# Kernel optimization log

Measured on AMD Instinct MI355X. Metric: run time of the kernel, lower is better.

Reference implementation:

```python
import jax, jax.numpy as jnp
import numpy as np

B, T, D = 1, 8192, 1024
H, DH = 16, 64
WIN = 128          # attention window (tokens on each side)
WB = 128
NB = T // WB
EPS = 1e-5


def _layernorm(x, g, b):
    mu = jnp.mean(x, axis=-1, keepdims=True)
    var = jnp.mean(jnp.square(x - mu), axis=-1, keepdims=True)
    return (x - mu) * jax.lax.rsqrt(var + EPS) * g + b


def _band_mask():
    # query offset i in [0, WB), key offset j in [0, 3*WB) within [prev|self|next] blocks
    i = jnp.arange(WB)[:, None]
    j = jnp.arange(3 * WB)[None, :]
    rel = j - WB - i                      # key_pos - query_pos
    band = jnp.abs(rel) <= WIN            # sliding window |i-j| <= W (matches torch mask)
    blk = jnp.arange(NB)[:, None, None]
    key_pos = blk * WB + (j - WB)[None]   # absolute key position
    return band[None] & (key_pos >= 0) & (key_pos < T)   # [NB, WB, 3*WB]


def _local_attention(q, k, v):
    # q,k,v: [B,H,T,DH] -> block-local SDPA, mathematically identical to
    # full SDPA with the additive band mask in the torch code.
    def blocks(t):
        return t.reshape(B, H, NB, WB, DH)
    qb = blocks(q)
    kp = jnp.pad(blocks(k), ((0, 0), (0, 0), (1, 1), (0, 0), (0, 0)))
    vp = jnp.pad(blocks(v), ((0, 0), (0, 0), (1, 1), (0, 0), (0, 0)))
    # gather [prev, self, next] key/value blocks: [B,H,NB,3*WB,DH]
    k3 = jnp.concatenate([kp[:, :, s:s + NB] for s in range(3)], axis=3)
    v3 = jnp.concatenate([vp[:, :, s:s + NB] for s in range(3)], axis=3)
    scores = jnp.einsum('bhnqd,bhnkd->bhnqk', qb, k3) / np.sqrt(DH).astype(np.float32)
    mask = _band_mask()                                   # [NB,WB,3WB]
    scores = jnp.where(mask[None, None], scores, -jnp.inf)
    attn = jax.nn.softmax(scores, axis=-1)
    out = jnp.einsum('bhnqk,bhnkd->bhnqd', attn, v3)      # [B,H,NB,WB,DH]
    return out.reshape(B, H, T, DH)


def setup_inputs() -> dict:
    key = jax.random.key(0)
    ks = jax.random.split(key, 7)
    s = 0.02
    return {
        'x': jax.random.normal(ks[0], (B, T, D), jnp.float32),
        'wq': jax.random.normal(ks[1], (D, D), jnp.float32) * s,
        'wk': jax.random.normal(ks[2], (D, D), jnp.float32) * s,
        'wv': jax.random.normal(ks[3], (D, D), jnp.float32) * s,
        'wo': jax.random.normal(ks[4], (D, D), jnp.float32) * s,
        'wg': jax.random.normal(ks[5], (D, 2 * D), jnp.float32) * s,
        'wd': jax.random.normal(ks[6], (2 * D, D), jnp.float32) * s,
        'norm_g': jnp.ones((D,), jnp.float32),
        'norm_b': jnp.zeros((D,), jnp.float32),
        'ffn_g': jnp.ones((D,), jnp.float32),
        'ffn_b': jnp.zeros((D,), jnp.float32),
    }


def reference(x, wq, wk, wv, wo, wg, wd, norm_g, norm_b, ffn_g, ffn_b):
    h = _layernorm(x, norm_g, norm_b)
    def heads(t):  # [B,T,D] -> [B,H,T,DH]
        return t.reshape(B, T, H, DH).transpose(0, 2, 1, 3)
    q, k, v = heads(h @ wq), heads(h @ wk), heads(h @ wv)
    attn_out = _local_attention(q, k, v)                     # [B,H,T,DH]
    attn_out = attn_out.transpose(0, 2, 1, 3).reshape(B, T, D)
    x = x + attn_out @ wo
    h = _layernorm(x, ffn_g, ffn_b)
    x = x + jax.nn.silu(h @ wg) @ wd
    return x
```

## Files before the change

### kernel.cpp

```cpp
#include <hip/hip_runtime.h>
#include <cstdint>

#define T_DIM 8192
#define D_DIM 1024
#define NB_DIM 64
#define QKS 2048

typedef __bf16 bf16x8 __attribute__((ext_vector_type(8)));
typedef __bf16 bf16x4 __attribute__((ext_vector_type(4)));
typedef float f32x4 __attribute__((ext_vector_type(4)));

#define MFMA16(a, b, c) __builtin_amdgcn_mfma_f32_16x16x32_bf16((a), (b), (c), 0, 0, 0)
#define BAR() asm volatile("s_barrier" ::: "memory")
#define VMCNT(n) asm volatile("s_waitcnt vmcnt(" #n ")" ::: "memory")

__device__ __forceinline__ void gld_lds16(const void* gsrc, void* ldst) {
  __builtin_amdgcn_global_load_lds(
      (__attribute__((address_space(1))) void*)(uintptr_t)gsrc,
      (__attribute__((address_space(3))) void*)(uintptr_t)ldst,
      16, 0, 0);
}

__global__ __launch_bounds__(256) void transpose_cvt(
    const float* __restrict__ W, __bf16* __restrict__ Wt, int K, int N) {
  __shared__ float tile[32][33];
  const int tx = threadIdx.x & 31, ty = threadIdx.x >> 5;
  const int n0 = blockIdx.x * 32, k0 = blockIdx.y * 32;
#pragma unroll
  for (int i = 0; i < 32; i += 8)
    tile[ty + i][tx] = W[(size_t)(k0 + ty + i) * N + n0 + tx];
  __syncthreads();
#pragma unroll
  for (int i = 0; i < 32; i += 8)
    Wt[(size_t)(n0 + ty + i) * K + k0 + tx] = (__bf16)tile[tx][ty + i];
}

template <typename TI>
__global__ __launch_bounds__(256) void ln_kernel(
    const TI* __restrict__ x, const float* __restrict__ g,
    const float* __restrict__ b, __bf16* __restrict__ out) {
  __shared__ float red[8];
  const int row = blockIdx.x, tid = threadIdx.x;
  float v0, v1, v2, v3;
  if constexpr (sizeof(TI) == 4) {
    const float4 v = ((const float4*)(x + (size_t)row * D_DIM))[tid];
    v0 = v.x; v1 = v.y; v2 = v.z; v3 = v.w;
  } else {
    const bf16x4 v = ((const bf16x4*)(x + (size_t)row * D_DIM))[tid];
    v0 = (float)v[0]; v1 = (float)v[1]; v2 = (float)v[2]; v3 = (float)v[3];
  }
  float s = v0 + v1 + v2 + v3;
#pragma unroll
  for (int off = 32; off >= 1; off >>= 1) s += __shfl_xor(s, off, 64);
  if ((tid & 63) == 0) red[tid >> 6] = s;
  __syncthreads();
  const float mean = (red[0] + red[1] + red[2] + red[3]) * (1.0f / D_DIM);
  const float d0 = v0 - mean, d1 = v1 - mean, d2 = v2 - mean, d3 = v3 - mean;
  float ss = d0 * d0 + d1 * d1 + d2 * d2 + d3 * d3;
#pragma unroll
  for (int off = 32; off >= 1; off >>= 1) ss += __shfl_xor(ss, off, 64);
  if ((tid & 63) == 0) red[4 + (tid >> 6)] = ss;
  __syncthreads();
  const float var = (red[4] + red[5] + red[6] + red[7]) * (1.0f / D_DIM);
  const float rstd = rsqrtf(var + 1e-5f);
  const float4 gg = ((const float4*)g)[tid];
  const float4 bb = ((const float4*)b)[tid];
  bf16x4 o;
  o[0] = (__bf16)(d0 * rstd * gg.x + bb.x);
  o[1] = (__bf16)(d1 * rstd * gg.y + bb.y);
  o[2] = (__bf16)(d2 * rstd * gg.z + bb.z);
  o[3] = (__bf16)(d3 * rstd * gg.w + bb.w);
  *(bf16x4*)(out + (size_t)row * D_DIM + tid * 4) = o;
}

__global__ __launch_bounds__(256, 2) void gemm_vt(
    const __bf16* __restrict__ A, const __bf16* __restrict__ Bt,
    __bf16* __restrict__ Cout, int M, int N, int K) {
  __shared__ __bf16 smem[32768];
  __bf16* As = smem;
  __bf16* Bs = smem + 16384;
  const int tid = threadIdx.x;
  const int l = tid & 63, w = tid >> 6;
  const int lr = l & 15, lg = l >> 4;
  const int wr = w >> 1, wc = w & 1;
  const int bm = blockIdx.y, bn = blockIdx.x;
  const size_t arow0 = (size_t)bm * 128;
  const size_t brow0 = (size_t)bn * 128;

  f32x4 acc[4][4];
  const f32x4 z4 = {0.f, 0.f, 0.f, 0.f};
#pragma unroll
  for (int m = 0; m < 4; ++m)
#pragma unroll
    for (int n = 0; n < 4; ++n) acc[m][n] = z4;

  auto stage = [&](int buf, int k0) {
#pragma unroll
    for (int r = 0; r < 4; ++r) {
      int ci = r * 256 + tid;
      int row = ci >> 3, c8 = ci & 7;
      gld_lds16(A + (arow0 + row) * K + k0 + c8 * 8, &As[buf * 8192 + ci * 8]);
    }
#pragma unroll
    for (int r = 0; r < 4; ++r) {
      int ci = r * 256 + tid;
      int row = ci >> 3, c8 = ci & 7;
      gld_lds16(Bt + (brow0 + row) * K + k0 + c8 * 8, &Bs[buf * 8192 + ci * 8]);
    }
  };

  stage(0, 0);
  const int nk = K >> 6;
  int cur = 0;
  __syncthreads();

  for (int t = 0; t < nk; ++t) {
    if (t + 1 < nk) stage(cur ^ 1, (t + 1) << 6);
#pragma unroll
    for (int kk = 0; kk < 2; ++kk) {
      bf16x8 af[4], bf_[4];
#pragma unroll
      for (int m = 0; m < 4; ++m)
        af[m] = *(const bf16x8*)&As[cur * 8192 + (wr * 64 + m * 16 + lr) * 64 + kk * 32 + lg * 8];
#pragma unroll
      for (int n = 0; n < 4; ++n)
        bf_[n] = *(const bf16x8*)&Bs[cur * 8192 + (wc * 64 + n * 16 + lr) * 64 + kk * 32 + lg * 8];
#pragma unroll
      for (int m = 0; m < 4; ++m)
#pragma unroll
        for (int n = 0; n < 4; ++n) acc[m][n] = MFMA16(af[m], bf_[n], acc[m][n]);
    }
    __syncthreads();
    cur ^= 1;
  }

  __bf16* Tt = smem;
#pragma unroll
  for (int m = 0; m < 4; ++m)
#pragma unroll
    for (int n = 0; n < 4; ++n)
#pragma unroll
      for (int r = 0; r < 4; ++r)
        Tt[(wc * 64 + n * 16 + lr) * 136 + wr * 64 + m * 16 + lg * 4 + r] =
            (__bf16)acc[m][n][r];
  __syncthreads();
#pragma unroll
  for (int i = 0; i < 8; ++i) {
    const int ci = i * 256 + tid;
    const int c = ci >> 4;
    const int rr = (ci & 15) * 8;
    const bf16x8 vv = *(const bf16x8*)&Tt[c * 136 + rr];
    *(bf16x8*)(Cout + (size_t)(bn * 128 + c) * M + bm * 128 + rr) = vv;
  }
}

template <int BM_, int EPI>
__global__ __launch_bounds__(512, 2) void gemm8(
    const __bf16* __restrict__ A, const __bf16* __restrict__ Bt,
    const void* __restrict__ Res, void* __restrict__ Cout,
    int M, int N, int K, int nbn) {
  constexpr int MF = BM_ / 32;
  constexpr int MH = MF / 2;
  constexpr int SA = 8 * MF;
  constexpr int LA = BM_ / 128;
  constexpr int ATILE = BM_ * 64;
  constexpr int AHALF = BM_ * 32;
  constexpr int BOFF = 2 * ATILE;
  __shared__ __bf16 lds[2 * BM_ * 64 + 32768];

  const int tid = threadIdx.x;
  const int l = tid & 63, w = tid >> 6;
  const int lr = l & 15, lg = l >> 4;
  const int wr = w >> 2, wc = w & 3;
  const int nwg = gridDim.x;
  const int bid = (int)blockIdx.x;
  const int swz = (bid & 7) * (nwg >> 3) + (bid >> 3);
  const int bm = swz / nbn, bn = swz % nbn;
  const int am0 = bm * BM_, bn0 = bn * 256;

  f32x4 acc[MF][4];
  const f32x4 z4 = {0.f, 0.f, 0.f, 0.f};
#pragma unroll
  for (int m = 0; m < MF; ++m)
#pragma unroll
    for (int n = 0; n < 4; ++n) acc[m][n] = z4;

  auto stageA = [&](int h, int b, int k0) {
#pragma unroll
    for (int r = 0; r < LA; ++r) {
      const int ci = r * 512 + tid;
      const int wri = ci >> 3, c8 = ci & 7;
      const int ra = (wri % SA) + (wri / SA) * (2 * SA) + h * SA;
      gld_lds16(A + (size_t)(am0 + ra) * K + k0 + ((c8 ^ (wri & 7)) << 3),
                (__bf16*)lds + b * ATILE + h * AHALF + ci * 8);
    }
  };
  auto stageB = [&](int h, int b, int k0) {
#pragma unroll
    for (int r = 0; r < 2; ++r) {
      const int ci = r * 512 + tid;
      const int wri = ci >> 3, c8 = ci & 7;
      const int rb = (wri & 31) + (wri >> 5) * 64 + h * 32;
      gld_lds16(Bt + (size_t)(bn0 + rb) * K + k0 + ((c8 ^ (wri & 7)) << 3),
                (__bf16*)lds + BOFF + b * 16384 + h * 8192 + ci * 8);
    }
  };

  const int x7 = lr & 7;
  const int aoff0 = (lr + wr * SA) * 64 + ((lg) ^ x7) * 8;
  const int aoff1 = (lr + wr * SA) * 64 + ((4 + lg) ^ x7) * 8;
  const int boff0 = BOFF + (lr + wc * 32) * 64 + ((lg) ^ x7) * 8;
  const int boff1 = BOFF + (lr + wc * 32) * 64 + ((4 + lg) ^ x7) * 8;

  const int nt = K >> 6;
  stageA(0, 0, 0);
  stageB(1, 0, 0);
  stageB(0, 0, 0);
  stageA(1, 0, 0);
  stageA(0, 1, 64);
  stageB(1, 1, 64);
  if constexpr (BM_ == 256) VMCNT(6); else VMCNT(4);
  BAR();

  int buf = 0;
  bf16x8 afr[MH][2], bfr0[2][2], bfr1[2][2];
  for (int t = 0; t < nt; ++t) {
    const bool s1 = (t + 1 < nt);
    const bool s2 = (t + 2 < nt);
    const int nb = buf ^ 1;
    const int k1 = (t + 1) << 6;
    const int k2 = (t + 2) << 6;
    const __bf16* pa0 = lds + buf * ATILE + aoff0;
    const __bf16* pa1 = lds + buf * ATILE + aoff1;
    const __bf16* pb0 = lds + buf * 16384 + boff0;
    const __bf16* pb1 = lds + buf * 16384 + boff1;

#pragma unroll
    for (int i = 0; i < MH; ++i) {
      afr[i][0] = *(const bf16x8*)(pa0 + i * 1024);
      afr[i][1] = *(const bf16x8*)(pa1 + i * 1024);
    }
#pragma unroll
    for (int j = 0; j < 2; ++j) {
      bfr0[j][0] = *(const bf16x8*)(pb0 + j * 1024);
      bfr0[j][1] = *(const bf16x8*)(pb1 + j * 1024);
    }
    if (s1) stageB(0, nb, k1);
    BAR();
    __builtin_amdgcn_s_setprio(1);
#pragma unroll
    for (int kk = 0; kk < 2; ++kk)
#pragma unroll
      for (int i = 0; i < MH; ++i)
#pragma unroll
        for (int j = 0; j < 2; ++j)
          acc[i][j] = MFMA16(afr[i][kk], bfr0[j][kk], acc[i][j]);
    __builtin_amdgcn_s_setprio(0);

#pragma unroll
    for (int j = 0; j < 2; ++j) {
      bfr1[j][0] = *(const bf16x8*)(pb0 + 8192 + j * 1024);
      bfr1[j][1] = *(const bf16x8*)(pb1 + 8192 + j * 1024);
    }
    if (s1) {
      stageA(1, nb, k1);
      if constexpr (BM_ == 256) VMCNT(8); else VMCNT(6);
    } else {
      VMCNT(0);
    }
    BAR();
    __builtin_amdgcn_s_setprio(1);
#pragma unroll
    for (int kk = 0; kk < 2; ++kk)
#pragma unroll
      for (int i = 0; i < MH; ++i)
#pragma unroll
        for (int j = 0; j < 2; ++j)
          acc[i][2 + j] = MFMA16(afr[i][kk], bfr1[j][kk], acc[i][2 + j]);
    __builtin_amdgcn_s_setprio(0);

#pragma unroll
    for (int i = 0; i < MH; ++i) {
      afr[i][0] = *(const bf16x8*)(pa0 + AHALF + i * 1024);
      afr[i][1] = *(const bf16x8*)(pa1 + AHALF + i * 1024);
    }
    if (s2) stageA(0, buf, k2);
    BAR();
    __builtin_amdgcn_s_setprio(1);
#pragma unroll
    for (int kk = 0; kk < 2; ++kk)
#pragma unroll
      for (int i = 0; i < MH; ++i)
#pragma unroll
        for (int j = 0; j < 2; ++j)
          acc[MH + i][2 + j] = MFMA16(afr[i][kk], bfr1[j][kk], acc[MH + i][2 + j]);
    __builtin_amdgcn_s_setprio(0);

    if (s2) {
      stageB(1, buf, k2);
      if constexpr (BM_ == 256) VMCNT(6); else VMCNT(4);
    } else if (s1) {
      if constexpr (BM_ == 256) VMCNT(2); else VMCNT(1);
    }
    BAR();
    __builtin_amdgcn_s_setprio(1);
#pragma unroll
    for (int kk = 0; kk < 2; ++kk)
#pragma unroll
      for (int i = 0; i < MH; ++i)
#pragma unroll
        for (int j = 0; j < 2; ++j)
          acc[MH + i][j] = MFMA16(afr[i][kk], bfr0[j][kk], acc[MH + i][j]);
    __builtin_amdgcn_s_setprio(0);

    buf = nb;
  }

  if constexpr (EPI == 5) {
    const __bf16* R = (const __bf16*)Res;
    float* O = (float*)Cout;
#pragma unroll
    for (int mf = 0; mf < MF; ++mf)
#pragma unroll
      for (int nf = 0; nf < 4; ++nf)
#pragma unroll
        for (int r = 0; r < 4; ++r) {
          const int row = am0 + wr * 2 * SA + mf * 16 + lg * 4 + r;
          const int col = bn0 + wc * 64 + nf * 16 + lr;
          const size_t idx = (size_t)row * N + col;
          O[idx] = acc[mf][nf][r] + (float)R[idx];
        }
  } else {
    __syncthreads();
    __bf16* Ct = (__bf16*)lds;
#pragma unroll
    for (int mf = 0; mf < MF; ++mf)
#pragma unroll
      for (int nf = 0; nf < 4; ++nf)
#pragma unroll
        for (int r = 0; r < 4; ++r) {
          const int rl = wr * 2 * SA + mf * 16 + lg * 4 + r;
          const int cl = wc * 64 + nf * 16 + lr;
          float v = acc[mf][nf][r];
          if constexpr (EPI == 3) v = v / (1.f + __expf(-v));
          if constexpr (EPI == 4)
            v += ((const float*)Res)[(size_t)(am0 + rl) * N + bn0 + cl];
          Ct[rl * 256 + (((cl >> 3) ^ (rl & 7)) << 3) + (cl & 7)] = (__bf16)v;
        }
    __syncthreads();
    __bf16* O = (__bf16*)Cout;
#pragma unroll
    for (int i = 0; i < BM_ / 16; ++i) {
      const int ci = i * 512 + tid;
      const int row = ci >> 5, c8 = ci & 31;
      *(bf16x8*)(O + (size_t)(am0 + row) * N + bn0 + c8 * 8) =
          *(const bf16x8*)&Ct[row * 256 + ((c8 ^ (row & 7)) << 3)];
    }
  }
}

__global__ __launch_bounds__(256, 2) void attn_kernel(
    const __bf16* __restrict__ qk, const __bf16* __restrict__ vT,
    __bf16* __restrict__ out) {
  __shared__ __bf16 Pl[4][32 * 136];

  const int tid = threadIdx.x;
  const int l = tid & 63, w = tid >> 6;
  const int lr = l & 15, lg = l >> 4;
  const int bx = (int)blockIdx.x;
  const int swz = (bx & 7) * 128 + (bx >> 3);
  const int h = swz >> 6;
  const int blk = swz & 63;
  __bf16* Pw = Pl[w];

  const __bf16* qbase =
      qk + (size_t)(blk * 128 + w * 32 + lr) * QKS + h * 64 + lg * 8;
  bf16x8 qf[2][2];
#pragma unroll
  for (int m = 0; m < 2; ++m)
#pragma unroll
    for (int ks = 0; ks < 2; ++ks)
      qf[m][ks] = *(const bf16x8*)(qbase + (size_t)m * 16 * QKS + ks * 32);

  const f32x4 z4 = {0.f, 0.f, 0.f, 0.f};
  float ssum[2][4];
  f32x4 o[2][4];
#pragma unroll
  for (int m = 0; m < 2; ++m) {
#pragma unroll
    for (int r = 0; r < 4; ++r) ssum[m][r] = 0.f;
#pragma unroll
    for (int n = 0; n < 4; ++n) o[m][n] = z4;
  }

  for (int it = 0; it < 3; ++it) {
    const int kb = blk + it - 1;
    if (kb < 0 || kb >= NB_DIM) continue;
    const int rel = it - 1;
    const int kclo = (rel < 0) ? (w * 2) : 0;
    const int kchi = (rel > 0) ? (w * 2 + 2) : 8;

    f32x4 s[2][8];
    const __bf16* kbase =
        qk + (size_t)(kb * 128 + lr) * QKS + 1024 + h * 64 + lg * 8;
#pragma unroll
    for (int kc = 0; kc < 8; ++kc) {
      if (kc < kclo || kc >= kchi) continue;
      const bf16x8 k0 = *(const bf16x8*)(kbase + (size_t)kc * 16 * QKS);
      const bf16x8 k1 = *(const bf16x8*)(kbase + (size_t)kc * 16 * QKS + 32);
      s[0][kc] = MFMA16(qf[0][0], k0, z4);
      s[1][kc] = MFMA16(qf[1][0], k0, z4);
      s[0][kc] = MFMA16(qf[0][1], k1, s[0][kc]);
      s[1][kc] = MFMA16(qf[1][1], k1, s[1][kc]);
    }

#pragma unroll
    for (int m = 0; m < 2; ++m) {
#pragma unroll
      for (int r = 0; r < 4; ++r) {
        const int qi = w * 32 + m * 16 + lg * 4 + r;
        float acc_s = 0.f;
#pragma unroll
        for (int kc = 0; kc < 8; ++kc) {
          if (kc < kclo || kc >= kchi) continue;
          const int kj = kc * 16 + lr;
          float p = __expf(s[m][kc][r] * 0.125f);
          const bool valid = (rel == 0) || (rel < 0 ? (kj >= qi) : (kj <= qi));
          p = valid ? p : 0.f;
          s[m][kc][r] = p;
          acc_s += p;
        }
        ssum[m][r] += acc_s;
      }
    }

#pragma unroll
    for (int m = 0; m < 2; ++m)
#pragma unroll
      for (int kc = 0; kc < 8; ++kc) {
        if (kc < kclo || kc >= kchi) continue;
#pragma unroll
        for (int r = 0; r < 4; ++r)
          Pw[(m * 16 + lg * 4 + r) * 136 + kc * 16 + lr] = (__bf16)s[m][kc][r];
      }

    const int kslo = kclo >> 1, kshi = kchi >> 1;
    const __bf16* vbase =
        vT + (size_t)(h * 64 + lr) * T_DIM + kb * 128 + lg * 8;
#pragma unroll
    for (int ks = 0; ks < 4; ++ks) {
      if (ks < kslo || ks >= kshi) continue;
      bf16x8 pa[2];
#pragma unroll
      for (int m = 0; m < 2; ++m)
        pa[m] = *(const bf16x8*)&Pw[(m * 16 + lr) * 136 + ks * 32 + lg * 8];
#pragma unroll
      for (int n = 0; n < 4; ++n) {
        const bf16x8 vb = *(const bf16x8*)(vbase + (size_t)n * 16 * T_DIM + ks * 32);
        o[0][n] = MFMA16(pa[0], vb, o[0][n]);
        o[1][n] = MFMA16(pa[1], vb, o[1][n]);
      }
    }
  }

  float inv[2][4];
#pragma unroll
  for (int m = 0; m < 2; ++m)
#pragma unroll
    for (int r = 0; r < 4; ++r) {
      float rs = ssum[m][r];
#pragma unroll
      for (int off = 1; off < 16; off <<= 1) rs += __shfl_xor(rs, off, 64);
      inv[m][r] = __builtin_amdgcn_rcpf(rs);
    }
#pragma unroll
  for (int m = 0; m < 2; ++m)
#pragma unroll
    for (int n = 0; n < 4; ++n)
#pragma unroll
      for (int r = 0; r < 4; ++r)
        Pw[(m * 16 + lg * 4 + r) * 136 + n * 16 + lr] =
            (__bf16)(o[m][n][r] * inv[m][r]);
#pragma unroll
  for (int i = 0; i < 4; ++i) {
    const int ci = i * 64 + l;
    const int qrow = ci >> 3;
    const int c8 = (ci & 7) * 8;
    const bf16x8 vv = *(const bf16x8*)&Pw[qrow * 136 + c8];
    *(bf16x8*)(out + (size_t)(blk * 128 + w * 32 + qrow) * D_DIM + h * 64 + c8) = vv;
  }
}

extern "C" void kernel_launch(void* const* d_in, const int* in_sizes, int n_in,
                              void* d_out, int out_size, void* d_ws, size_t ws_size,
                              hipStream_t stream) {
  (void)in_sizes; (void)n_in; (void)out_size; (void)ws_size;
  const float* x      = (const float*)d_in[0];
  const float* wq     = (const float*)d_in[1];
  const float* wk     = (const float*)d_in[2];
  const float* wv     = (const float*)d_in[3];
  const float* wo     = (const float*)d_in[4];
  const float* wg     = (const float*)d_in[5];
  const float* wd     = (const float*)d_in[6];
  const float* norm_g = (const float*)d_in[7];
  const float* norm_b = (const float*)d_in[8];
  const float* ffn_g  = (const float*)d_in[9];
  const float* ffn_b  = (const float*)d_in[10];
  float* out = (float*)d_out;

  char* ws = (char*)d_ws;
  constexpr size_t MB = 1ull << 20;
  __bf16* wqkT = (__bf16*)(ws + 0 * MB);
  __bf16* wvT  = (__bf16*)(ws + 4 * MB);
  __bf16* woT  = (__bf16*)(ws + 6 * MB);
  __bf16* wgT  = (__bf16*)(ws + 8 * MB);
  __bf16* wdT  = (__bf16*)(ws + 12 * MB);
  __bf16* hbuf = (__bf16*)(ws + 16 * MB);
  __bf16* qkbf = (__bf16*)(ws + 32 * MB);
  __bf16* gbf  = (__bf16*)(ws + 32 * MB);
  __bf16* vTbf = (__bf16*)(ws + 64 * MB);
  __bf16* x2bf = (__bf16*)(ws + 80 * MB);

  transpose_cvt<<<dim3(32, 32), 256, 0, stream>>>(wq, wqkT, 1024, 1024);
  transpose_cvt<<<dim3(32, 32), 256, 0, stream>>>(wk, wqkT + 1024 * 1024, 1024, 1024);
  transpose_cvt<<<dim3(32, 32), 256, 0, stream>>>(wv, wvT, 1024, 1024);
  transpose_cvt<<<dim3(32, 32), 256, 0, stream>>>(wo, woT, 1024, 1024);
  transpose_cvt<<<dim3(64, 32), 256, 0, stream>>>(wg, wgT, 1024, 2048);
  transpose_cvt<<<dim3(32, 64), 256, 0, stream>>>(wd, wdT, 2048, 1024);

  ln_kernel<float><<<8192, 256, 0, stream>>>(x, norm_g, norm_b, hbuf);

  gemm8<256, 0><<<256, 512, 0, stream>>>(hbuf, wqkT, nullptr, qkbf, 8192, 2048, 1024, 8);
  gemm_vt<<<dim3(8, 64), 256, 0, stream>>>(hbuf, wvT, vTbf, 8192, 1024, 1024);

  attn_kernel<<<1024, 256, 0, stream>>>(qkbf, vTbf, hbuf);

  gemm8<128, 4><<<256, 512, 0, stream>>>(hbuf, woT, x, x2bf, 8192, 1024, 1024, 4);

  ln_kernel<__bf16><<<8192, 256, 0, stream>>>(x2bf, ffn_g, ffn_b, hbuf);

  gemm8<256, 3><<<256, 512, 0, stream>>>(hbuf, wgT, nullptr, gbf, 8192, 2048, 1024, 8);

  gemm8<128, 5><<<256, 512, 0, stream>>>(gbf, wdT, x2bf, out, 8192, 1024, 2048, 4);
}
```

Before: 255.4 us.

## Fuse weight transposes into one launch and split wide GEMMs into BM=128 halves

Replaces six weight transpose-convert launches with one kernel that picks the source matrix from the block index. Drops the BM=256 GEMM variant: the QK and gate projections (N=2048) now run as two BM=128 launches over column halves, with a separate output leading dimension. This cuts launch overhead and the 256-row tile's register and LDS pressure, at the cost of an extra launch per wide GEMM and less A-tile reuse across N.

Measured after the change: 259.8 us. No clear change (+1.7%).

```diff
diff --git a/kernel.cpp b/kernel.cpp
--- a/kernel.cpp
+++ b/kernel.cpp
@@ -21,11 +21,25 @@
       16, 0, 0);
 }
 
-__global__ __launch_bounds__(256) void transpose_cvt(
-    const float* __restrict__ W, __bf16* __restrict__ Wt, int K, int N) {
+__global__ __launch_bounds__(256) void transpose_all(
+    const float* __restrict__ wq, const float* __restrict__ wk,
+    const float* __restrict__ wv, const float* __restrict__ wo,
+    const float* __restrict__ wg, const float* __restrict__ wd,
+    __bf16* __restrict__ wqkT, __bf16* __restrict__ wvT,
+    __bf16* __restrict__ woT, __bf16* __restrict__ wgT,
+    __bf16* __restrict__ wdT) {
   __shared__ float tile[32][33];
+  const int bid = (int)blockIdx.x;
+  const float* W; __bf16* Wt; int K, N, n0, k0, local;
+  if (bid < 1024)      { W = wq; Wt = wqkT;            K = 1024; N = 1024; local = bid; }
+  else if (bid < 2048) { W = wk; Wt = wqkT + 1048576;  K = 1024; N = 1024; local = bid - 1024; }
+  else if (bid < 3072) { W = wv; Wt = wvT;             K = 1024; N = 1024; local = bid - 2048; }
+  else if (bid < 4096) { W = wo; Wt = woT;             K = 1024; N = 1024; local = bid - 3072; }
+  else if (bid < 6144) { W = wg; Wt = wgT;             K = 1024; N = 2048; local = bid - 4096; }
+  else                 { W = wd; Wt = wdT;             K = 2048; N = 1024; local = bid - 6144; }
+  if (N == 2048) { n0 = (local & 63) * 32; k0 = (local >> 6) * 32; }
+  else           { n0 = (local & 31) * 32; k0 = (local >> 5) * 32; }
   const int tx = threadIdx.x & 31, ty = threadIdx.x >> 5;
-  const int n0 = blockIdx.x * 32, k0 = blockIdx.y * 32;
 #pragma unroll
   for (int i = 0; i < 32; i += 8)
     tile[ty + i][tx] = W[(size_t)(k0 + ty + i) * N + n0 + tx];
@@ -154,11 +168,12 @@
   }
 }
 
-template <int BM_, int EPI>
+template <int EPI>
 __global__ __launch_bounds__(512, 2) void gemm8(
     const __bf16* __restrict__ A, const __bf16* __restrict__ Bt,
     const void* __restrict__ Res, void* __restrict__ Cout,
-    int M, int N, int K, int nbn) {
+    int M, int K, int nbn, int ldc) {
+  constexpr int BM_ = 128;
   constexpr int MF = BM_ / 32;
   constexpr int MH = MF / 2;
   constexpr int SA = 8 * MF;
@@ -219,7 +234,7 @@
   stageA(1, 0, 0);
   stageA(0, 1, 64);
   stageB(1, 1, 64);
-  if constexpr (BM_ == 256) VMCNT(6); else VMCNT(4);
+  VMCNT(4);
   BAR();
 
   int buf = 0;
@@ -264,7 +279,7 @@
     }
     if (s1) {
       stageA(1, nb, k1);
-      if constexpr (BM_ == 256) VMCNT(8); else VMCNT(6);
+      VMCNT(6);
     } else {
       VMCNT(0);
     }
@@ -298,9 +313,9 @@
 
     if (s2) {
       stageB(1, buf, k2);
-      if constexpr (BM_ == 256) VMCNT(6); else VMCNT(4);
+      VMCNT(4);
     } else if (s1) {
-      if constexpr (BM_ == 256) VMCNT(2); else VMCNT(1);
+      VMCNT(1);
     }
     BAR();
     __builtin_amdgcn_s_setprio(1);
@@ -327,7 +342,7 @@
         for (int r = 0; r < 4; ++r) {
           const int row = am0 + wr * 2 * SA + mf * 16 + lg * 4 + r;
           const int col = bn0 + wc * 64 + nf * 16 + lr;
-          const size_t idx = (size_t)row * N + col;
+          const size_t idx = (size_t)row * ldc + col;
           O[idx] = acc[mf][nf][r] + (float)R[idx];
         }
   } else {
@@ -344,7 +359,7 @@
           float v = acc[mf][nf][r];
           if constexpr (EPI == 3) v = v / (1.f + __expf(-v));
           if constexpr (EPI == 4)
-            v += ((const float*)Res)[(size_t)(am0 + rl) * N + bn0 + cl];
+            v += ((const float*)Res)[(size_t)(am0 + rl) * D_DIM + bn0 + cl];
           Ct[rl * 256 + (((cl >> 3) ^ (rl & 7)) << 3) + (cl & 7)] = (__bf16)v;
         }
     __syncthreads();
@@ -353,7 +368,7 @@
     for (int i = 0; i < BM_ / 16; ++i) {
       const int ci = i * 512 + tid;
       const int row = ci >> 5, c8 = ci & 31;
-      *(bf16x8*)(O + (size_t)(am0 + row) * N + bn0 + c8 * 8) =
+      *(bf16x8*)(O + (size_t)(am0 + row) * ldc + bn0 + c8 * 8) =
           *(const bf16x8*)&Ct[row * 256 + ((c8 ^ (row & 7)) << 3)];
     }
   }
@@ -521,25 +536,27 @@
   __bf16* vTbf = (__bf16*)(ws + 64 * MB);
   __bf16* x2bf = (__bf16*)(ws + 80 * MB);
 
-  transpose_cvt<<<dim3(32, 32), 256, 0, stream>>>(wq, wqkT, 1024, 1024);
-  transpose_cvt<<<dim3(32, 32), 256, 0, stream>>>(wk, wqkT + 1024 * 1024, 1024, 1024);
-  transpose_cvt<<<dim3(32, 32), 256, 0, stream>>>(wv, wvT, 1024, 1024);
-  transpose_cvt<<<dim3(32, 32), 256, 0, stream>>>(wo, woT, 1024, 1024);
-  transpose_cvt<<<dim3(64, 32), 256, 0, stream>>>(wg, wgT, 1024, 2048);
-  transpose_cvt<<<dim3(32, 64), 256, 0, stream>>>(wd, wdT, 2048, 1024);
+  transpose_all<<<8192, 256, 0, stream>>>(wq, wk, wv, wo, wg, wd,
+                                          wqkT, wvT, woT, wgT, wdT);
 
   ln_kernel<float><<<8192, 256, 0, stream>>>(x, norm_g, norm_b, hbuf);
 
-  gemm8<256, 0><<<256, 512, 0, stream>>>(hbuf, wqkT, nullptr, qkbf, 8192, 2048, 1024, 8);
+  gemm8<0><<<256, 512, 0, stream>>>(hbuf, wqkT, nullptr, qkbf,
+                                    8192, 1024, 4, 2048);
+  gemm8<0><<<256, 512, 0, stream>>>(hbuf, wqkT + 1024 * 1024, nullptr, qkbf + 1024,
+                                    8192, 1024, 4, 2048);
   gemm_vt<<<dim3(8, 64), 256, 0, stream>>>(hbuf, wvT, vTbf, 8192, 1024, 1024);
 
   attn_kernel<<<1024, 256, 0, stream>>>(qkbf, vTbf, hbuf);
 
-  gemm8<128, 4><<<256, 512, 0, stream>>>(hbuf, woT, x, x2bf, 8192, 1024, 1024, 4);
+  gemm8<4><<<256, 512, 0, stream>>>(hbuf, woT, x, x2bf, 8192, 1024, 4, 1024);
 
   ln_kernel<__bf16><<<8192, 256, 0, stream>>>(x2bf, ffn_g, ffn_b, hbuf);
 
-  gemm8<256, 3><<<256, 512, 0, stream>>>(hbuf, wgT, nullptr, gbf, 8192, 2048, 1024, 8);
-
-  gemm8<128, 5><<<256, 512, 0, stream>>>(gbf, wdT, x2bf, out, 8192, 1024, 2048, 4);
-}
+  gemm8<3><<<256, 512, 0, stream>>>(hbuf, wgT, nullptr, gbf,
+                                    8192, 1024, 4, 2048);
+  gemm8<3><<<256, 512, 0, stream>>>(hbuf, wgT + 1024 * 1024, nullptr, gbf + 1024,
+                                    8192, 1024, 4, 2048);
+
+  gemm8<5><<<256, 512, 0, stream>>>(gbf, wdT, x2bf, out, 8192, 2048, 4, 1024);
+}
```

## Merge weight transposes into one launch and compute V^T via gemm8 with swapped operands

Applied to the files above, without the earlier changes.

Six separate transpose_cvt launches become a single transpose_all kernel that dispatches on block index, which cuts launch overhead. The dedicated gemm_vt kernel, which transposed V through LDS in its epilogue, is removed. V^T is now produced by the existing tuned gemm8<128,0> kernel, computing Wv^T·h^T by passing wvT as A and hbuf as Bt. This reuses the faster 512-thread GEMM path, but relies on gemm8 handling M=1024 and N=8192 with 32 column blocks correctly.

After: 245.4 us. 1.04x faster.

```diff
diff --git a/kernel.cpp b/kernel.cpp
--- a/kernel.cpp
+++ b/kernel.cpp
@@ -21,11 +21,25 @@
       16, 0, 0);
 }
 
-__global__ __launch_bounds__(256) void transpose_cvt(
-    const float* __restrict__ W, __bf16* __restrict__ Wt, int K, int N) {
+__global__ __launch_bounds__(256) void transpose_all(
+    const float* __restrict__ wq, const float* __restrict__ wk,
+    const float* __restrict__ wv, const float* __restrict__ wo,
+    const float* __restrict__ wg, const float* __restrict__ wd,
+    __bf16* __restrict__ wqkT, __bf16* __restrict__ wvT,
+    __bf16* __restrict__ woT, __bf16* __restrict__ wgT,
+    __bf16* __restrict__ wdT) {
   __shared__ float tile[32][33];
+  const int bid = (int)blockIdx.x;
+  const float* W; __bf16* Wt; int K, N, n0, k0, local;
+  if (bid < 1024)      { W = wq; Wt = wqkT;            K = 1024; N = 1024; local = bid; }
+  else if (bid < 2048) { W = wk; Wt = wqkT + 1048576;  K = 1024; N = 1024; local = bid - 1024; }
+  else if (bid < 3072) { W = wv; Wt = wvT;             K = 1024; N = 1024; local = bid - 2048; }
+  else if (bid < 4096) { W = wo; Wt = woT;             K = 1024; N = 1024; local = bid - 3072; }
+  else if (bid < 6144) { W = wg; Wt = wgT;             K = 1024; N = 2048; local = bid - 4096; }
+  else                 { W = wd; Wt = wdT;             K = 2048; N = 1024; local = bid - 6144; }
+  if (N == 2048) { n0 = (local & 63) * 32; k0 = (local >> 6) * 32; }
+  else           { n0 = (local & 31) * 32; k0 = (local >> 5) * 32; }
   const int tx = threadIdx.x & 31, ty = threadIdx.x >> 5;
-  const int n0 = blockIdx.x * 32, k0 = blockIdx.y * 32;
 #pragma unroll
   for (int i = 0; i < 32; i += 8)
     tile[ty + i][tx] = W[(size_t)(k0 + ty + i) * N + n0 + tx];
@@ -71,87 +85,6 @@
   o[2] = (__bf16)(d2 * rstd * gg.z + bb.z);
   o[3] = (__bf16)(d3 * rstd * gg.w + bb.w);
   *(bf16x4*)(out + (size_t)row * D_DIM + tid * 4) = o;
-}
-
-__global__ __launch_bounds__(256, 2) void gemm_vt(
-    const __bf16* __restrict__ A, const __bf16* __restrict__ Bt,
-    __bf16* __restrict__ Cout, int M, int N, int K) {
-  __shared__ __bf16 smem[32768];
-  __bf16* As = smem;
-  __bf16* Bs = smem + 16384;
-  const int tid = threadIdx.x;
-  const int l = tid & 63, w = tid >> 6;
-  const int lr = l & 15, lg = l >> 4;
-  const int wr = w >> 1, wc = w & 1;
-  const int bm = blockIdx.y, bn = blockIdx.x;
-  const size_t arow0 = (size_t)bm * 128;
-  const size_t brow0 = (size_t)bn * 128;
-
-  f32x4 acc[4][4];
-  const f32x4 z4 = {0.f, 0.f, 0.f, 0.f};
-#pragma unroll
-  for (int m = 0; m < 4; ++m)
-#pragma unroll
-    for (int n = 0; n < 4; ++n) acc[m][n] = z4;
-
-  auto stage = [&](int buf, int k0) {
-#pragma unroll
-    for (int r = 0; r < 4; ++r) {
-      int ci = r * 256 + tid;
-      int row = ci >> 3, c8 = ci & 7;
-      gld_lds16(A + (arow0 + row) * K + k0 + c8 * 8, &As[buf * 8192 + ci * 8]);
-    }
-#pragma unroll
-    for (int r = 0; r < 4; ++r) {
-      int ci = r * 256 + tid;
-      int row = ci >> 3, c8 = ci & 7;
-      gld_lds16(Bt + (brow0 + row) * K + k0 + c8 * 8, &Bs[buf * 8192 + ci * 8]);
-    }
-  };
-
-  stage(0, 0);
-  const int nk = K >> 6;
-  int cur = 0;
-  __syncthreads();
-
-  for (int t = 0; t < nk; ++t) {
-    if (t + 1 < nk) stage(cur ^ 1, (t + 1) << 6);
-#pragma unroll
-    for (int kk = 0; kk < 2; ++kk) {
-      bf16x8 af[4], bf_[4];
-#pragma unroll
-      for (int m = 0; m < 4; ++m)
-        af[m] = *(const bf16x8*)&As[cur * 8192 + (wr * 64 + m * 16 + lr) * 64 + kk * 32 + lg * 8];
-#pragma unroll
-      for (int n = 0; n < 4; ++n)
-        bf_[n] = *(const bf16x8*)&Bs[cur * 8192 + (wc * 64 + n * 16 + lr) * 64 + kk * 32 + lg * 8];
-#pragma unroll
-      for (int m = 0; m < 4; ++m)
-#pragma unroll
-        for (int n = 0; n < 4; ++n) acc[m][n] = MFMA16(af[m], bf_[n], acc[m][n]);
-    }
-    __syncthreads();
-    cur ^= 1;
-  }
-
-  __bf16* Tt = smem;
-#pragma unroll
-  for (int m = 0; m < 4; ++m)
-#pragma unroll
-    for (int n = 0; n < 4; ++n)
-#pragma unroll
-      for (int r = 0; r < 4; ++r)
-        Tt[(wc * 64 + n * 16 + lr) * 136 + wr * 64 + m * 16 + lg * 4 + r] =
-            (__bf16)acc[m][n][r];
-  __syncthreads();
-#pragma unroll
-  for (int i = 0; i < 8; ++i) {
-    const int ci = i * 256 + tid;
-    const int c = ci >> 4;
-    const int rr = (ci & 15) * 8;
-    const bf16x8 vv = *(const bf16x8*)&Tt[c * 136 + rr];
-    *(bf16x8*)(Cout + (size_t)(bn * 128 + c) * M + bm * 128 + rr) = vv;
-  }
 }
 
 template <int BM_, int EPI>
@@ -521,17 +454,15 @@
   __bf16* vTbf = (__bf16*)(ws + 64 * MB);
   __bf16* x2bf = (__bf16*)(ws + 80 * MB);
 
-  transpose_cvt<<<dim3(32, 32), 256, 0, stream>>>(wq, wqkT, 1024, 1024);
-  transpose_cvt<<<dim3(32, 32), 256, 0, stream>>>(wk, wqkT + 1024 * 1024, 1024, 1024);
-  transpose_cvt<<<dim3(32, 32), 256, 0, stream>>>(wv, wvT, 1024, 1024);
-  transpose_cvt<<<dim3(32, 32), 256, 0, stream>>>(wo, woT, 1024, 1024);
-  transpose_cvt<<<dim3(64, 32), 256, 0, stream>>>(wg, wgT, 1024, 2048);
-  transpose_cvt<<<dim3(32, 64), 256, 0, stream>>>(wd, wdT, 2048, 1024);
+  transpose_all<<<8192, 256, 0, stream>>>(wq, wk, wv, wo, wg, wd,
+                                          wqkT, wvT, woT, wgT, wdT);
 
   ln_kernel<float><<<8192, 256, 0, stream>>>(x, norm_g, norm_b, hbuf);
 
-  gemm8<256, 0><<<256, 512, 0, stream>>>(hbuf, wqkT, nullptr, qkbf, 8192, 2048, 1024, 8);
-  gemm_vt<<<dim3(8, 64), 256, 0, stream>>>(hbuf, wvT, vTbf, 8192, 1024, 1024);
+  gemm8<256, 0><<<256, 512, 0, stream>>>(hbuf, wqkT, nullptr, qkbf,
+                                         8192, 2048, 1024, 8);
+  gemm8<128, 0><<<256, 512, 0, stream>>>(wvT, hbuf, nullptr, vTbf,
+                                         1024, 8192, 1024, 32);
 
   attn_kernel<<<1024, 256, 0, stream>>>(qkbf, vTbf, hbuf);
 
@@ -539,7 +470,8 @@
 
   ln_kernel<__bf16><<<8192, 256, 0, stream>>>(x2bf, ffn_g, ffn_b, hbuf);
 
-  gemm8<256, 3><<<256, 512, 0, stream>>>(hbuf, wgT, nullptr, gbf, 8192, 2048, 1024, 8);
+  gemm8<256, 3><<<256, 512, 0, stream>>>(hbuf, wgT, nullptr, gbf,
+                                         8192, 2048, 1024, 8);
 
   gemm8<128, 5><<<256, 512, 0, stream>>>(gbf, wdT, x2bf, out, 8192, 1024, 2048, 4);
 }
```
